# Kernel tuning notes

Measured on AMD Instinct MI355X. Metric: run time of the kernel, lower is better.

The kernel has to match this reference:

```python
import jax, jax.numpy as jnp
import numpy as np

B, C, H, W = 16, 64, 64, 64
C1, C2 = 8, 32  # block_channels_1 = C/8, block_channels_2 = C/2


def _conv1x1(x, w, b):
    # x: [B,C,H,W], w: [O,C] (1x1 kernel), b: [O]
    return jnp.einsum('bchw,oc->bohw', x, w) + b[None, :, None, None]


def _maxpool2(x):
    # MaxPool2d(kernel_size=2): window 2x2, stride 2, no padding
    return jax.lax.reduce_window(x, -jnp.inf, jax.lax.max,
                                 (1, 1, 2, 2), (1, 1, 2, 2), 'VALID')


def setup_inputs() -> dict:
    key = jax.random.key(0)
    ks = jax.random.split(key, 10)
    s = lambda fan_in: 1.0 / np.sqrt(fan_in)
    return {
        'nonlocal_input': jax.random.normal(ks[0], (B, C, H, W), jnp.float32),
        # spectral-normalized conv weights are treated as the effective (already
        # normalized) weights; 1x1 kernels stored as [out, in]
        'w_delta': jax.random.normal(ks[1], (C1, C), jnp.float32) * s(C),
        'b_delta': jax.random.normal(ks[2], (C1,), jnp.float32) * 0.01,
        'w_phi': jax.random.normal(ks[3], (C1, C), jnp.float32) * s(C),
        'b_phi': jax.random.normal(ks[4], (C1,), jnp.float32) * 0.01,
        'w_g': jax.random.normal(ks[5], (C2, C), jnp.float32) * s(C),
        'b_g': jax.random.normal(ks[6], (C2,), jnp.float32) * 0.01,
        'w_last': jax.random.normal(ks[7], (C, C2), jnp.float32) * s(C2),
        'b_last': jax.random.normal(ks[8], (C,), jnp.float32) * 0.01,
        # torch init is zeros; use a nonzero value so the attention path matters
        'gamma': jnp.asarray([0.7], jnp.float32),
    }


def reference(nonlocal_input, w_delta, b_delta, w_phi, b_phi, w_g, b_g,
              w_last, b_last, gamma):
    x = nonlocal_input
    b, c, h, w = x.shape

    # delta: [B,C1,H,W] -> [B, HW, C1]
    delta = _conv1x1(x, w_delta, b_delta)
    delta = jnp.transpose(delta, (0, 2, 3, 1)).reshape(b, h * w, C1)

    # phi: conv + pool -> [B,C1,H/2,W/2]; NOTE: the original permutes
    # (1,0,2,3) BEFORE reshaping to [B, C1, HW/4] (faithful to source).
    phi = _maxpool2(_conv1x1(x, w_phi, b_phi))
    phi = jnp.transpose(phi, (1, 0, 2, 3)).reshape(b, C1, -1)

    # attention: [B, HW, HW/4]
    attn = jax.nn.softmax(jnp.einsum('bnk,bkm->bnm', delta, phi), axis=-1)

    # g: conv + pool -> [B, HW/4, C2]
    g = _maxpool2(_conv1x1(x, w_g, b_g))
    g = jnp.transpose(g, (0, 2, 3, 1)).reshape(b, -1, C2)

    out = jnp.einsum('bnm,bmc->bnc', attn, g)          # [B, HW, C2]
    out = out.reshape(b, h, w, C2).transpose(0, 3, 1, 2)  # [B, C2, H, W]

    return gamma[0] * _conv1x1(out, w_last, b_last) + x
```

## Files before the change

kernel.cpp:

```cpp
#include <hip/hip_runtime.h>
#include <hip/hip_bf16.h>
#include <math.h>

typedef __attribute__((ext_vector_type(8))) short bf16x8;
typedef __attribute__((ext_vector_type(4))) float f32x4;

#define B_   16
#define C_   64
#define C1_  8
#define C2_  32
#define HW_  4096
#define M_   1024
#define LOG2E 1.4426950408889634f
#define MFMA_BF16 __builtin_amdgcn_mfma_f32_16x16x32_bf16

__device__ __forceinline__ unsigned short f2bf(float f) {
  union { float f; unsigned u; } v; v.f = f;
  unsigned r = (v.u + 0x7fffu + ((v.u >> 16) & 1u)) >> 16;
  return (unsigned short)r;
}
__device__ __forceinline__ float bf2f(unsigned short h) {
  union { unsigned u; float f; } v; v.u = ((unsigned)h) << 16;
  return v.f;
}

__global__ __launch_bounds__(256, 4)
void k_pre(const float* __restrict__ x,
           const float* __restrict__ w_phi, const float* __restrict__ b_phi,
           const float* __restrict__ w_g,   const float* __restrict__ b_g,
           unsigned short* __restrict__ phi_s,
           unsigned short* __restrict__ g_t) {
  __shared__ float comb[2*64*41];
  int tid = threadIdx.x;

  int qt  = tid >> 6;
  int sub = tid & 63;
  int id  = blockIdx.x * 64 + sub;
  int pix = id & 3;
  int pm  = id >> 2;
  int b = pm >> 10;
  int m = pm & 1023;
  int py = 2*(m >> 5) + (pix >> 1);
  int px = 2*(m & 31) + (pix & 1);
  int n = py * 64 + px;

  int c0 = __builtin_amdgcn_readfirstlane(qt << 4);

  const float* xp = x + ((size_t)b*C_ + c0)*HW_ + n;
  float xv[16];
  #pragma unroll
  for (int i = 0; i < 16; ++i) xv[i] = xp[(size_t)i * HW_];

  float ap[8], ag[32];
  #pragma unroll
  for (int o = 0; o < 8; ++o) {
    const float* wp = w_phi + o*C_ + c0;
    float a = 0.f;
    #pragma unroll
    for (int i = 0; i < 16; ++i) a += xv[i]*wp[i];
    ap[o] = a;
  }
  #pragma unroll
  for (int o = 0; o < 32; ++o) {
    const float* wg = w_g + o*C_ + c0;
    float a = 0.f;
    #pragma unroll
    for (int i = 0; i < 16; ++i) a += xv[i]*wg[i];
    ag[o] = a;
  }

  if (qt == 1 || qt == 3) {
    float* cb = comb + (((qt >> 1)*64) + sub)*41;
    #pragma unroll
    for (int o = 0; o < 8; ++o) cb[o] = ap[o];
    #pragma unroll
    for (int o = 0; o < 32; ++o) cb[8+o] = ag[o];
  }
  __syncthreads();
  if (qt == 0 || qt == 2) {
    const float* cb = comb + (((qt >> 1)*64) + sub)*41;
    #pragma unroll
    for (int o = 0; o < 8; ++o) ap[o] += cb[o];
    #pragma unroll
    for (int o = 0; o < 32; ++o) ag[o] += cb[8+o];
  }
  __syncthreads();
  if (qt == 2) {
    float* cb = comb + sub*41;
    #pragma unroll
    for (int o = 0; o < 8; ++o) cb[o] = ap[o];
    #pragma unroll
    for (int o = 0; o < 32; ++o) cb[8+o] = ag[o];
  }
  __syncthreads();
  if (qt == 0) {
    const float* cb = comb + sub*41;
    #pragma unroll
    for (int o = 0; o < 8; ++o) ap[o] += cb[o];
    #pragma unroll
    for (int o = 0; o < 32; ++o) ag[o] += cb[8+o];

    #pragma unroll
    for (int o = 0; o < 8; ++o) {
      float v = ap[o];
      v = fmaxf(v, __shfl_xor(v, 1));
      v = fmaxf(v, __shfl_xor(v, 2));
      ap[o] = v;
    }
    #pragma unroll
    for (int o = 0; o < 32; ++o) {
      float v = ag[o];
      v = fmaxf(v, __shfl_xor(v, 1));
      v = fmaxf(v, __shfl_xor(v, 2));
      ag[o] = v;
    }

    if ((sub & 3) == 0) {
      #pragma unroll
      for (int cp = 0; cp < 8; ++cp) {
        int f = cp*16 + b;
        float v = ap[cp] + b_phi[cp];
        unsigned short hi = f2bf(v);
        unsigned short* pr = phi_s + ((size_t)(f >> 3)*M_ + m)*16;
        pr[f & 7]       = hi;
        pr[8 + (f & 7)] = f2bf(v - bf2f(hi));
      }
      #pragma unroll
      for (int o = 0; o < 32; ++o)
        g_t[((size_t)b*C2_ + o)*M_ + m] = f2bf(ag[o] + b_g[o]);
    }
  }
}

__global__ __launch_bounds__(512, 4)
void k_attn(const float* __restrict__ x,
            const float* __restrict__ w_delta,
            const float* __restrict__ b_delta,
            const unsigned short* __restrict__ phi_s,
            const unsigned short* __restrict__ g_t,
            const float* __restrict__ w_last,
            const float* __restrict__ b_last,
            const float* __restrict__ gamma,
            float* __restrict__ out) {
  __shared__ __align__(16) unsigned char lds_raw[50176];
  __shared__ __align__(8)  unsigned short delta_lds[128*16];
  unsigned short* phi_lds = (unsigned short*)lds_raw;
  unsigned short* g_lds   = (unsigned short*)(lds_raw + 16384);
  float* o_sh = (float*)lds_raw;
  float* cmb  = (float*)(lds_raw + 16896);

  int tid  = threadIdx.x;
  int lane = tid & 63;
  int wv   = tid >> 6;
  int rg   = wv & 3;
  int kh   = wv >> 2;
  int r    = lane & 15;
  int q    = lane >> 4;
  int bx = blockIdx.x;
  int b  = bx >> 5;
  int n0 = (bx & 31) * 128;

  {
    int row  = tid & 127;
    int cp2  = __builtin_amdgcn_readfirstlane(tid >> 7);
    const float* wd0 = w_delta + (2*cp2)   * C_;
    const float* wd1 = w_delta + (2*cp2+1) * C_;
    const float* xr  = x + (size_t)b*C_*HW_ + n0 + row;
    float a0 = 0.f, a1 = 0.f;
    #pragma unroll
    for (int c = 0; c < C_; ++c) {
      float v = xr[(size_t)c * HW_];
      a0 += v * wd0[c];
      a1 += v * wd1[c];
    }
    a0 = (a0 + b_delta[2*cp2])   * LOG2E;
    a1 = (a1 + b_delta[2*cp2+1]) * LOG2E;
    unsigned short h0 = f2bf(a0), h1 = f2bf(a1);
    unsigned short l0 = f2bf(a0 - bf2f(h0)), l1 = f2bf(a1 - bf2f(h1));
    *(unsigned*)(delta_lds + row*16 + 2*cp2)     = (unsigned)h0 | ((unsigned)h1 << 16);
    *(unsigned*)(delta_lds + row*16 + 8 + 2*cp2) = (unsigned)l0 | ((unsigned)l1 << 16);
  }
  __syncthreads();

  bf16x8 df[2];
  #pragma unroll
  for (int t = 0; t < 2; ++t)
    df[t] = *(const bf16x8*)(delta_lds + (rg*32 + t*16 + r)*16 + (q & 1)*8);

  int phi_off = (q >> 1) * 8;
  int key0 = (r >> 2)*8 + (r & 3);
  int key1 = key0 + 4;

  bf16x8 ones;
  #pragma unroll
  for (int i = 0; i < 8; ++i) ones[i] = (short)0x3F80;

  f32x4 acc[2][2];
  f32x4 den[2];
  f32x4 zero = {0,0,0,0};
  #pragma unroll
  for (int t = 0; t < 2; ++t) { acc[t][0] = zero; acc[t][1] = zero; den[t] = zero; }

  for (int p = 0; p < 2; ++p) {
    if (p) __syncthreads();
    {
      const uint4* psrc = (const uint4*)(phi_s + ((size_t)b*M_ + p*512)*16);
      uint4* pdst = (uint4*)phi_lds;
      #pragma unroll
      for (int u = 0; u < 2; ++u) pdst[tid + u*512] = psrc[tid + u*512];
      #pragma unroll
      for (int u = 0; u < 4; ++u) {
        int uu = tid + u*512;
        int c2 = uu >> 6, pos = uu & 63;
        *(uint4*)(g_lds + c2*520 + pos*8) =
            *(const uint4*)(g_t + ((size_t)b*C2_ + c2)*M_ + p*512 + pos*8);
      }
    }
    __syncthreads();

    #pragma unroll 2
    for (int kc = 0; kc < 256; kc += 32) {
      int kl = kh*256 + kc;
      bf16x8 aphi0 = *(const bf16x8*)(phi_lds + (size_t)(kl + key0)*16 + phi_off);
      bf16x8 aphi1 = *(const bf16x8*)(phi_lds + (size_t)(kl + key1)*16 + phi_off);
      bf16x8 bg0   = *(const bf16x8*)(g_lds + r*520        + kl + q*8);
      bf16x8 bg1   = *(const bf16x8*)(g_lds + (16 + r)*520 + kl + q*8);

      #pragma unroll
      for (int t = 0; t < 2; ++t) {
        f32x4 s0 = MFMA_BF16(aphi0, df[t], zero, 0, 0, 0);
        f32x4 s1 = MFMA_BF16(aphi1, df[t], zero, 0, 0, 0);
        union { bf16x8 v; __hip_bfloat162 h[4]; } e;
        e.h[0] = __float22bfloat162_rn(make_float2(__builtin_amdgcn_exp2f(s0[0]),
                                                   __builtin_amdgcn_exp2f(s0[1])));
        e.h[1] = __float22bfloat162_rn(make_float2(__builtin_amdgcn_exp2f(s0[2]),
                                                   __builtin_amdgcn_exp2f(s0[3])));
        e.h[2] = __float22bfloat162_rn(make_float2(__builtin_amdgcn_exp2f(s1[0]),
                                                   __builtin_amdgcn_exp2f(s1[1])));
        e.h[3] = __float22bfloat162_rn(make_float2(__builtin_amdgcn_exp2f(s1[2]),
                                                   __builtin_amdgcn_exp2f(s1[3])));
        acc[t][0] = MFMA_BF16(e.v, bg0, acc[t][0], 0, 0, 0);
        acc[t][1] = MFMA_BF16(e.v, bg1, acc[t][1], 0, 0, 0);
        den[t]    = MFMA_BF16(e.v, ones, den[t], 0, 0, 0);
      }
    }
  }

  __syncthreads();
  if (kh == 1) {
    #pragma unroll
    for (int t = 0; t < 2; ++t) {
      #pragma unroll
      for (int reg = 0; reg < 4; ++reg) {
        int row = rg*32 + t*16 + q*4 + reg;
        cmb[row*34 + r]      = acc[t][0][reg];
        cmb[row*34 + 16 + r] = acc[t][1][reg];
        if (r == 0) cmb[row*34 + 32] = den[t][reg];
      }
    }
  }
  __syncthreads();
  if (kh == 0) {
    #pragma unroll
    for (int t = 0; t < 2; ++t) {
      #pragma unroll
      for (int reg = 0; reg < 4; ++reg) {
        int row = rg*32 + t*16 + q*4 + reg;
        float o0 = acc[t][0][reg] + cmb[row*34 + r];
        float o1 = acc[t][1][reg] + cmb[row*34 + 16 + r];
        float dn = den[t][reg]    + cmb[row*34 + 32];
        float iv = __builtin_amdgcn_rcpf(dn);
        o_sh[row*33 + r]      = o0 * iv;
        o_sh[row*33 + 16 + r] = o1 * iv;
      }
    }
  }
  __syncthreads();

  int rr  = tid & 127;
  int wqu = __builtin_amdgcn_readfirstlane(tid >> 7);
  float o_reg[32];
  #pragma unroll
  for (int c = 0; c < 32; ++c) o_reg[c] = o_sh[rr*33 + c];
  float gm = gamma[0];
  for (int i = 0; i < 16; ++i) {
    int co = wqu*16 + i;
    const float* wl = w_last + co*32;
    float a = b_last[co];
    #pragma unroll
    for (int c = 0; c < 32; ++c) a += wl[c] * o_reg[c];
    size_t oi = ((size_t)b*C_ + co)*HW_ + (size_t)(n0 + rr);
    out[oi] = gm * a + x[oi];
  }
}

extern "C" void kernel_launch(void* const* d_in, const int* in_sizes, int n_in,
                              void* d_out, int out_size, void* d_ws, size_t ws_size,
                              hipStream_t stream) {
  const float* x       = (const float*)d_in[0];
  const float* w_delta = (const float*)d_in[1];
  const float* b_delta = (const float*)d_in[2];
  const float* w_phi   = (const float*)d_in[3];
  const float* b_phi   = (const float*)d_in[4];
  const float* w_g     = (const float*)d_in[5];
  const float* b_g     = (const float*)d_in[6];
  const float* w_last  = (const float*)d_in[7];
  const float* b_last  = (const float*)d_in[8];
  const float* gamma   = (const float*)d_in[9];
  float* out = (float*)d_out;

  unsigned short* ws = (unsigned short*)d_ws;
  unsigned short* phi_s = ws;
  unsigned short* g_t   = ws + (size_t)B_*M_*16;

  hipLaunchKernelGGL(k_pre, dim3(1024), dim3(256), 0, stream,
                     x, w_phi, b_phi, w_g, b_g, phi_s, g_t);
  hipLaunchKernelGGL(k_attn, dim3(512), dim3(512), 0, stream,
                     x, w_delta, b_delta, phi_s, g_t, w_last, b_last, gamma, out);
}
```

Measured before the change: 114.7 us.

## Compute delta projection in pre-pass kernel and load it from workspace

The delta 1x1 conv moves from the attention kernel into k_pre, which already reads every x pixel for phi and g. It is stored as hi/lo bf16 pairs in a new workspace buffer. The attention kernel now loads its delta fragments straight from global memory, which removes a second full read of x, the per-block dot products, an LDS buffer and a barrier. The cost is extra registers and LDS in k_pre (comb grows) and an extra global write and read of the delta buffer.

```diff
diff --git a/kernel.cpp b/kernel.cpp
--- a/kernel.cpp
+++ b/kernel.cpp
@@ -26,11 +26,13 @@
 
 __global__ __launch_bounds__(256, 4)
 void k_pre(const float* __restrict__ x,
+           const float* __restrict__ w_delta, const float* __restrict__ b_delta,
            const float* __restrict__ w_phi, const float* __restrict__ b_phi,
            const float* __restrict__ w_g,   const float* __restrict__ b_g,
+           unsigned short* __restrict__ delta_s,
            unsigned short* __restrict__ phi_s,
            unsigned short* __restrict__ g_t) {
-  __shared__ float comb[2*64*41];
+  __shared__ float comb[2*64*49];
   int tid = threadIdx.x;
 
   int qt  = tid >> 6;
@@ -51,7 +53,15 @@
   #pragma unroll
   for (int i = 0; i < 16; ++i) xv[i] = xp[(size_t)i * HW_];
 
-  float ap[8], ag[32];
+  float ad[8], ap[8], ag[32];
+  #pragma unroll
+  for (int o = 0; o < 8; ++o) {
+    const float* wd = w_delta + o*C_ + c0;
+    float a = 0.f;
+    #pragma unroll
+    for (int i = 0; i < 16; ++i) a += xv[i]*wd[i];
+    ad[o] = a;
+  }
   #pragma unroll
   for (int o = 0; o < 8; ++o) {
     const float* wp = w_phi + o*C_ + c0;
@@ -70,35 +80,57 @@
   }
 
   if (qt == 1 || qt == 3) {
-    float* cb = comb + (((qt >> 1)*64) + sub)*41;
-    #pragma unroll
-    for (int o = 0; o < 8; ++o) cb[o] = ap[o];
-    #pragma unroll
-    for (int o = 0; o < 32; ++o) cb[8+o] = ag[o];
+    float* cb = comb + (((qt >> 1)*64) + sub)*49;
+    #pragma unroll
+    for (int o = 0; o < 8; ++o) cb[o] = ad[o];
+    #pragma unroll
+    for (int o = 0; o < 8; ++o) cb[8+o] = ap[o];
+    #pragma unroll
+    for (int o = 0; o < 32; ++o) cb[16+o] = ag[o];
   }
   __syncthreads();
   if (qt == 0 || qt == 2) {
-    const float* cb = comb + (((qt >> 1)*64) + sub)*41;
-    #pragma unroll
-    for (int o = 0; o < 8; ++o) ap[o] += cb[o];
-    #pragma unroll
-    for (int o = 0; o < 32; ++o) ag[o] += cb[8+o];
+    const float* cb = comb + (((qt >> 1)*64) + sub)*49;
+    #pragma unroll
+    for (int o = 0; o < 8; ++o) ad[o] += cb[o];
+    #pragma unroll
+    for (int o = 0; o < 8; ++o) ap[o] += cb[8+o];
+    #pragma unroll
+    for (int o = 0; o < 32; ++o) ag[o] += cb[16+o];
   }
   __syncthreads();
   if (qt == 2) {
-    float* cb = comb + sub*41;
-    #pragma unroll
-    for (int o = 0; o < 8; ++o) cb[o] = ap[o];
-    #pragma unroll
-    for (int o = 0; o < 32; ++o) cb[8+o] = ag[o];
+    float* cb = comb + sub*49;
+    #pragma unroll
+    for (int o = 0; o < 8; ++o) cb[o] = ad[o];
+    #pragma unroll
+    for (int o = 0; o < 8; ++o) cb[8+o] = ap[o];
+    #pragma unroll
+    for (int o = 0; o < 32; ++o) cb[16+o] = ag[o];
   }
   __syncthreads();
   if (qt == 0) {
-    const float* cb = comb + sub*41;
-    #pragma unroll
-    for (int o = 0; o < 8; ++o) ap[o] += cb[o];
-    #pragma unroll
-    for (int o = 0; o < 32; ++o) ag[o] += cb[8+o];
+    const float* cb = comb + sub*49;
+    #pragma unroll
+    for (int o = 0; o < 8; ++o) ad[o] += cb[o];
+    #pragma unroll
+    for (int o = 0; o < 8; ++o) ap[o] += cb[8+o];
+    #pragma unroll
+    for (int o = 0; o < 32; ++o) ag[o] += cb[16+o];
+
+    {
+      union { unsigned short s[8]; uint4 v; } dh, dl;
+      #pragma unroll
+      for (int o = 0; o < 8; ++o) {
+        float v = (ad[o] + b_delta[o]) * LOG2E;
+        unsigned short hi = f2bf(v);
+        dh.s[o] = hi;
+        dl.s[o] = f2bf(v - bf2f(hi));
+      }
+      uint4* dp = (uint4*)(delta_s + ((size_t)b*HW_ + n)*16);
+      dp[0] = dh.v;
+      dp[1] = dl.v;
+    }
 
     #pragma unroll
     for (int o = 0; o < 8; ++o) {
@@ -134,8 +166,7 @@
 
 __global__ __launch_bounds__(512, 4)
 void k_attn(const float* __restrict__ x,
-            const float* __restrict__ w_delta,
-            const float* __restrict__ b_delta,
+            const unsigned short* __restrict__ delta_s,
             const unsigned short* __restrict__ phi_s,
             const unsigned short* __restrict__ g_t,
             const float* __restrict__ w_last,
@@ -143,7 +174,6 @@
             const float* __restrict__ gamma,
             float* __restrict__ out) {
   __shared__ __align__(16) unsigned char lds_raw[50176];
-  __shared__ __align__(8)  unsigned short delta_lds[128*16];
   unsigned short* phi_lds = (unsigned short*)lds_raw;
   unsigned short* g_lds   = (unsigned short*)(lds_raw + 16384);
   float* o_sh = (float*)lds_raw;
@@ -160,32 +190,13 @@
   int b  = bx >> 5;
   int n0 = (bx & 31) * 128;
 
+  bf16x8 df[2];
   {
-    int row  = tid & 127;
-    int cp2  = __builtin_amdgcn_readfirstlane(tid >> 7);
-    const float* wd0 = w_delta + (2*cp2)   * C_;
-    const float* wd1 = w_delta + (2*cp2+1) * C_;
-    const float* xr  = x + (size_t)b*C_*HW_ + n0 + row;
-    float a0 = 0.f, a1 = 0.f;
-    #pragma unroll
-    for (int c = 0; c < C_; ++c) {
-      float v = xr[(size_t)c * HW_];
-      a0 += v * wd0[c];
-      a1 += v * wd1[c];
-    }
-    a0 = (a0 + b_delta[2*cp2])   * LOG2E;
-    a1 = (a1 + b_delta[2*cp2+1]) * LOG2E;
-    unsigned short h0 = f2bf(a0), h1 = f2bf(a1);
-    unsigned short l0 = f2bf(a0 - bf2f(h0)), l1 = f2bf(a1 - bf2f(h1));
-    *(unsigned*)(delta_lds + row*16 + 2*cp2)     = (unsigned)h0 | ((unsigned)h1 << 16);
-    *(unsigned*)(delta_lds + row*16 + 8 + 2*cp2) = (unsigned)l0 | ((unsigned)l1 << 16);
-  }
-  __syncthreads();
-
-  bf16x8 df[2];
-  #pragma unroll
-  for (int t = 0; t < 2; ++t)
-    df[t] = *(const bf16x8*)(delta_lds + (rg*32 + t*16 + r)*16 + (q & 1)*8);
+    const unsigned short* dp =
+        delta_s + ((size_t)b*HW_ + n0 + rg*32 + r)*16 + (q & 1)*8;
+    df[0] = *(const bf16x8*)(dp);
+    df[1] = *(const bf16x8*)(dp + 16*16);
+  }
 
   int phi_off = (q >> 1) * 8;
   int key0 = (r >> 2)*8 + (r & 3);
@@ -310,11 +321,13 @@
   float* out = (float*)d_out;
 
   unsigned short* ws = (unsigned short*)d_ws;
-  unsigned short* phi_s = ws;
-  unsigned short* g_t   = ws + (size_t)B_*M_*16;
+  unsigned short* phi_s   = ws;
+  unsigned short* g_t     = ws + (size_t)B_*M_*16;
+  unsigned short* delta_s = ws + (size_t)B_*M_*16 + (size_t)B_*C2_*M_;
 
   hipLaunchKernelGGL(k_pre, dim3(1024), dim3(256), 0, stream,
-                     x, w_phi, b_phi, w_g, b_g, phi_s, g_t);
+                     x, w_delta, b_delta, w_phi, b_phi, w_g, b_g,
+                     delta_s, phi_s, g_t);
   hipLaunchKernelGGL(k_attn, dim3(512), dim3(512), 0, stream,
-                     x, w_delta, b_delta, phi_s, g_t, w_last, b_last, gamma, out);
-}
+                     x, delta_s, phi_s, g_t, w_last, b_last, gamma, out);
+}
```

Result: no change. 112.9 us (median of 2 runs) (-1.6%).
